# Kernel tuning notes

Hardware: AMD Instinct MI355X
Metric: run time of the kernel (lower is better)

## Reference

```python
import jax, jax.numpy as jnp
import numpy as np

LN_EPS = 1e-5
FACTOR = 4

def layer_norm(x, w, b):
    mu = jnp.mean(x, axis=-1, keepdims=True)
    var = jnp.mean((x - mu) ** 2, axis=-1, keepdims=True)
    return (x - mu) * jax.lax.rsqrt(var + LN_EPS) * w + b

def setup_inputs() -> dict:
    key = jax.random.key(0)
    k1, k2, k3 = jax.random.split(key, 3)
    B, Sq, Skv, D = 4, 2048, 8192, 1024
    return {
        "query": jax.random.normal(k1, (B, Sq, D), dtype=jnp.float32),
        "key": jax.random.normal(k2, (B, Skv, D), dtype=jnp.float32),
        "value": jax.random.normal(k3, (B, Skv, D), dtype=jnp.float32),
        "ln_weight": jnp.ones((D,), dtype=jnp.float32),
        "ln_bias": jnp.zeros((D,), dtype=jnp.float32),
    }

def attention_downsampling(q, k, v, factor):
    # q: [B, S//f, D], k/v: [B, S, D]
    B, S, D = k.shape
    k_win = k.reshape(B, S // factor, factor, D)
    weights = jnp.einsum('bsd,bsfd->bsf', q, k_win).reshape(B, S)  # no softmax
    attn = weights[:, :, None] * v                                  # [B, S, D]
    attn = attn.reshape(B, S // factor, factor, D).sum(axis=2)      # [B, S//f, D]
    return attn

def reference(query, key, value, ln_weight, ln_bias):
    # pre-norm (post_norm=False): residual + attention over normed q/k/v
    qn = layer_norm(query, ln_weight, ln_bias)
    kn = layer_norm(key, ln_weight, ln_bias)
    vn = layer_norm(value, ln_weight, ln_bias)
    return query + attention_downsampling(qn, kn, vn, FACTOR)
```

## Files before the change

kernel.cpp:

```cpp
#include <hip/hip_runtime.h>


constexpr int D      = 1024;
constexpr int FACTOR = 4;
constexpr int BLOCK  = 256;
constexpr int NW     = BLOCK / 64;
constexpr float EPS  = 1e-5f;

__device__ __forceinline__ float wave_reduce_sum(float x) {
#pragma unroll
    for (int off = 32; off > 0; off >>= 1)
        x += __shfl_down(x, off, 64);
    return x;
}

template <int N>
__device__ __forceinline__ void block_reduce(float* vals, float* s_buf) {
    const int lane = threadIdx.x & 63;
    const int wave = threadIdx.x >> 6;
#pragma unroll
    for (int i = 0; i < N; i++) {
        float x = wave_reduce_sum(vals[i]);
        if (lane == 0) s_buf[wave * N + i] = x;
    }
    __syncthreads();
#pragma unroll
    for (int i = 0; i < N; i++) {
        float t = 0.f;
#pragma unroll
        for (int w = 0; w < NW; w++) t += s_buf[w * N + i];
        vals[i] = t;
    }
    __syncthreads();
}

__device__ __forceinline__ float4 ln4(float4 x, float mu, float rs, float4 w, float4 b) {
    float4 r;
    r.x = (x.x - mu) * rs * w.x + b.x;
    r.y = (x.y - mu) * rs * w.y + b.y;
    r.z = (x.z - mu) * rs * w.z + b.z;
    r.w = (x.w - mu) * rs * w.w + b.w;
    return r;
}

__device__ __forceinline__ float dot4(float4 a, float4 b) {
    return a.x * b.x + a.y * b.y + a.z * b.z + a.w * b.w;
}

__global__ __launch_bounds__(BLOCK) void attn_ds_kernel(
    const float* __restrict__ q,
    const float* __restrict__ k,
    const float* __restrict__ v,
    const float* __restrict__ lw,
    const float* __restrict__ lb,
    float* __restrict__ out)
{
    __shared__ float s_buf[NW * 18];

    const size_t row = blockIdx.x;
    const int tid = threadIdx.x;
    const int d0  = tid * 4;

    const float4 qv = *(const float4*)(q + row * D + d0);
    float4 kv[FACTOR], vv[FACTOR];
#pragma unroll
    for (int f = 0; f < FACTOR; f++) {
        kv[f] = *(const float4*)(k + (row * FACTOR + f) * (size_t)D + d0);
        vv[f] = *(const float4*)(v + (row * FACTOR + f) * (size_t)D + d0);
    }
    const float4 wv = *(const float4*)(lw + d0);
    const float4 bv = *(const float4*)(lb + d0);

    float red[18];
    red[0] = qv.x + qv.y + qv.z + qv.w;
    red[1] = qv.x * qv.x + qv.y * qv.y + qv.z * qv.z + qv.w * qv.w;
#pragma unroll
    for (int f = 0; f < FACTOR; f++) {
        red[2 + 2 * f]  = kv[f].x + kv[f].y + kv[f].z + kv[f].w;
        red[3 + 2 * f]  = kv[f].x * kv[f].x + kv[f].y * kv[f].y + kv[f].z * kv[f].z + kv[f].w * kv[f].w;
        red[10 + 2 * f] = vv[f].x + vv[f].y + vv[f].z + vv[f].w;
        red[11 + 2 * f] = vv[f].x * vv[f].x + vv[f].y * vv[f].y + vv[f].z * vv[f].z + vv[f].w * vv[f].w;
    }
    block_reduce<18>(red, s_buf);

    const float invD = 1.0f / (float)D;
    const float mu_q = red[0] * invD;
    const float rs_q = rsqrtf(red[1] * invD - mu_q * mu_q + EPS);
    float mu_k[FACTOR], rs_k[FACTOR], mu_v[FACTOR], rs_v[FACTOR];
#pragma unroll
    for (int f = 0; f < FACTOR; f++) {
        mu_k[f] = red[2 + 2 * f] * invD;
        rs_k[f] = rsqrtf(red[3 + 2 * f] * invD - mu_k[f] * mu_k[f] + EPS);
        mu_v[f] = red[10 + 2 * f] * invD;
        rs_v[f] = rsqrtf(red[11 + 2 * f] * invD - mu_v[f] * mu_v[f] + EPS);
    }

    const float4 qn = ln4(qv, mu_q, rs_q, wv, bv);
    float dp[FACTOR];
#pragma unroll
    for (int f = 0; f < FACTOR; f++) {
        const float4 kn = ln4(kv[f], mu_k[f], rs_k[f], wv, bv);
        dp[f] = dot4(qn, kn);
    }
    block_reduce<FACTOR>(dp, s_buf);

    float4 acc = qv;
#pragma unroll
    for (int f = 0; f < FACTOR; f++) {
        const float4 vn = ln4(vv[f], mu_v[f], rs_v[f], wv, bv);
        acc.x += dp[f] * vn.x;
        acc.y += dp[f] * vn.y;
        acc.z += dp[f] * vn.z;
        acc.w += dp[f] * vn.w;
    }
    *(float4*)(out + row * D + d0) = acc;
}

extern "C" void kernel_launch(void* const* d_in, const int* in_sizes, int n_in,
                              void* d_out, int out_size, void* d_ws, size_t ws_size,
                              hipStream_t stream) {
    const float* q  = (const float*)d_in[0];
    const float* k  = (const float*)d_in[1];
    const float* v  = (const float*)d_in[2];
    const float* lw = (const float*)d_in[3];
    const float* lb = (const float*)d_in[4];
    float* out = (float*)d_out;

    const int rows = in_sizes[0] / D;
    attn_ds_kernel<<<dim3(rows), dim3(BLOCK), 0, stream>>>(q, k, v, lw, lb, out);
}
```

Before: 310.4 us.

## Process one row per wave with DPP reductions and algebraic LN-dot expansion

Each wave now handles a full output row, so block-level shared-memory reductions and barriers are replaced with DPP-based wave reductions. The normalized q·k dot product is computed from raw moment sums (sum, sum of squares, weighted cross terms) instead of materializing normalized vectors. V loads are deferred until after the K statistics are reduced to limit register pressure. The trade-off is much higher per-thread register use, the occupancy hint may cause spills, and the expanded variance formula carries some cancellation risk.

```diff
diff --git a/kernel.cpp b/kernel.cpp
--- a/kernel.cpp
+++ b/kernel.cpp
@@ -1,53 +1,28 @@
 #include <hip/hip_runtime.h>
 
 
-constexpr int D      = 1024;
-constexpr int FACTOR = 4;
-constexpr int BLOCK  = 256;
-constexpr int NW     = BLOCK / 64;
-constexpr float EPS  = 1e-5f;
+constexpr int D     = 1024;
+constexpr int BLOCK = 256;
+constexpr float EPS = 1e-5f;
 
-__device__ __forceinline__ float wave_reduce_sum(float x) {
-#pragma unroll
-    for (int off = 32; off > 0; off >>= 1)
-        x += __shfl_down(x, off, 64);
-    return x;
+template<int CTRL>
+__device__ __forceinline__ float dpp_add(float x) {
+    int xi = __builtin_bit_cast(int, x);
+    int yi = __builtin_amdgcn_update_dpp(0, xi, CTRL, 0xF, 0xF, true);
+    return x + __builtin_bit_cast(float, yi);
 }
 
-template <int N>
-__device__ __forceinline__ void block_reduce(float* vals, float* s_buf) {
-    const int lane = threadIdx.x & 63;
-    const int wave = threadIdx.x >> 6;
-#pragma unroll
-    for (int i = 0; i < N; i++) {
-        float x = wave_reduce_sum(vals[i]);
-        if (lane == 0) s_buf[wave * N + i] = x;
-    }
-    __syncthreads();
-#pragma unroll
-    for (int i = 0; i < N; i++) {
-        float t = 0.f;
-#pragma unroll
-        for (int w = 0; w < NW; w++) t += s_buf[w * N + i];
-        vals[i] = t;
-    }
-    __syncthreads();
+__device__ __forceinline__ float wave_sum(float x) {
+    x = dpp_add<0x111>(x);
+    x = dpp_add<0x112>(x);
+    x = dpp_add<0x114>(x);
+    x = dpp_add<0x118>(x);
+    x = dpp_add<0x142>(x);
+    x = dpp_add<0x143>(x);
+    return __builtin_bit_cast(float, __builtin_amdgcn_readlane(__builtin_bit_cast(int, x), 63));
 }
 
-__device__ __forceinline__ float4 ln4(float4 x, float mu, float rs, float4 w, float4 b) {
-    float4 r;
-    r.x = (x.x - mu) * rs * w.x + b.x;
-    r.y = (x.y - mu) * rs * w.y + b.y;
-    r.z = (x.z - mu) * rs * w.z + b.z;
-    r.w = (x.w - mu) * rs * w.w + b.w;
-    return r;
-}
-
-__device__ __forceinline__ float dot4(float4 a, float4 b) {
-    return a.x * b.x + a.y * b.y + a.z * b.z + a.w * b.w;
-}
-
-__global__ __launch_bounds__(BLOCK) void attn_ds_kernel(
+__global__ __launch_bounds__(BLOCK, 3) void attn_ds_kernel(
     const float* __restrict__ q,
     const float* __restrict__ k,
     const float* __restrict__ v,
@@ -55,65 +30,127 @@
     const float* __restrict__ lb,
     float* __restrict__ out)
 {
-    __shared__ float s_buf[NW * 18];
+    const int lane = threadIdx.x & 63;
+    const int wid  = threadIdx.x >> 6;
+    const long row = (long)blockIdx.x * 4 + wid;
+    const int off0 = lane * 4;
 
-    const size_t row = blockIdx.x;
-    const int tid = threadIdx.x;
-    const int d0  = tid * 4;
+    const float* qp = q + row * D;
+    const float* kp = k + row * (4L * D);
+    const float* vp = v + row * (4L * D);
 
-    const float4 qv = *(const float4*)(q + row * D + d0);
-    float4 kv[FACTOR], vv[FACTOR];
+    float4 qv[4], wv[4], bv[4], kv[4][4];
 #pragma unroll
-    for (int f = 0; f < FACTOR; f++) {
-        kv[f] = *(const float4*)(k + (row * FACTOR + f) * (size_t)D + d0);
-        vv[f] = *(const float4*)(v + (row * FACTOR + f) * (size_t)D + d0);
+    for (int c = 0; c < 4; c++) {
+        const int e = c * 256 + off0;
+        qv[c] = *(const float4*)(qp + e);
+        wv[c] = *(const float4*)(lw + e);
+        bv[c] = *(const float4*)(lb + e);
     }
-    const float4 wv = *(const float4*)(lw + d0);
-    const float4 bv = *(const float4*)(lb + d0);
+#pragma unroll
+    for (int f = 0; f < 4; f++)
+#pragma unroll
+        for (int c = 0; c < 4; c++)
+            kv[f][c] = *(const float4*)(kp + f * D + c * 256 + off0);
 
-    float red[18];
-    red[0] = qv.x + qv.y + qv.z + qv.w;
-    red[1] = qv.x * qv.x + qv.y * qv.y + qv.z * qv.z + qv.w * qv.w;
+    float4 qw[4];
+    float Sq = 0, Sqq = 0, Sq_w2 = 0, Sq_wb = 0, Sw2 = 0, Swb = 0, Sbb = 0;
 #pragma unroll
-    for (int f = 0; f < FACTOR; f++) {
-        red[2 + 2 * f]  = kv[f].x + kv[f].y + kv[f].z + kv[f].w;
-        red[3 + 2 * f]  = kv[f].x * kv[f].x + kv[f].y * kv[f].y + kv[f].z * kv[f].z + kv[f].w * kv[f].w;
-        red[10 + 2 * f] = vv[f].x + vv[f].y + vv[f].z + vv[f].w;
-        red[11 + 2 * f] = vv[f].x * vv[f].x + vv[f].y * vv[f].y + vv[f].z * vv[f].z + vv[f].w * vv[f].w;
+    for (int c = 0; c < 4; c++) {
+#define ACCQ(m) { \
+        float qe = qv[c].m, we = wv[c].m, be = bv[c].m; \
+        float qwe = qe * we; qw[c].m = qwe; \
+        Sq += qe; Sqq = fmaf(qe, qe, Sqq); \
+        Sq_w2 = fmaf(qwe, we, Sq_w2); Sq_wb = fmaf(qwe, be, Sq_wb); \
+        Sw2 = fmaf(we, we, Sw2); Swb = fmaf(we, be, Swb); Sbb = fmaf(be, be, Sbb); }
+        ACCQ(x) ACCQ(y) ACCQ(z) ACCQ(w)
+#undef ACCQ
     }
-    block_reduce<18>(red, s_buf);
+
+    float Sk[4], Skk[4], Sk_w2[4], Sk_wb[4], Sqk[4];
+#pragma unroll
+    for (int f = 0; f < 4; f++) {
+        float s0 = 0, s1 = 0, s2 = 0, s3 = 0, s4 = 0;
+#pragma unroll
+        for (int c = 0; c < 4; c++) {
+#define ACCK(m) { \
+            float ke = kv[f][c].m, we = wv[c].m, be = bv[c].m; \
+            float kwe = ke * we; \
+            s0 += ke; s1 = fmaf(ke, ke, s1); \
+            s2 = fmaf(kwe, we, s2); s3 = fmaf(kwe, be, s3); \
+            s4 = fmaf(qw[c].m, kwe, s4); }
+            ACCK(x) ACCK(y) ACCK(z) ACCK(w)
+#undef ACCK
+        }
+        Sk[f] = s0; Skk[f] = s1; Sk_w2[f] = s2; Sk_wb[f] = s3; Sqk[f] = s4;
+    }
+
+    Sq = wave_sum(Sq);   Sqq = wave_sum(Sqq);
+    Sq_w2 = wave_sum(Sq_w2); Sq_wb = wave_sum(Sq_wb);
+    Sw2 = wave_sum(Sw2); Swb = wave_sum(Swb); Sbb = wave_sum(Sbb);
+#pragma unroll
+    for (int f = 0; f < 4; f++) {
+        Sk[f] = wave_sum(Sk[f]);       Skk[f] = wave_sum(Skk[f]);
+        Sk_w2[f] = wave_sum(Sk_w2[f]); Sk_wb[f] = wave_sum(Sk_wb[f]);
+        Sqk[f] = wave_sum(Sqk[f]);
+    }
+
+    asm volatile("" ::: "memory");
+    float4 vv[4][4];
+#pragma unroll
+    for (int f = 0; f < 4; f++)
+#pragma unroll
+        for (int c = 0; c < 4; c++)
+            vv[f][c] = *(const float4*)(vp + f * D + c * 256 + off0);
 
     const float invD = 1.0f / (float)D;
-    const float mu_q = red[0] * invD;
-    const float rs_q = rsqrtf(red[1] * invD - mu_q * mu_q + EPS);
-    float mu_k[FACTOR], rs_k[FACTOR], mu_v[FACTOR], rs_v[FACTOR];
+    const float mu_q = Sq * invD;
+    const float rs_q = rsqrtf(fmaf(-mu_q, mu_q, Sqq * invD) + EPS);
+    const float qwb_c = Sq_wb - mu_q * Swb;
+    float dp[4];
 #pragma unroll
-    for (int f = 0; f < FACTOR; f++) {
-        mu_k[f] = red[2 + 2 * f] * invD;
-        rs_k[f] = rsqrtf(red[3 + 2 * f] * invD - mu_k[f] * mu_k[f] + EPS);
-        mu_v[f] = red[10 + 2 * f] * invD;
-        rs_v[f] = rsqrtf(red[11 + 2 * f] * invD - mu_v[f] * mu_v[f] + EPS);
+    for (int f = 0; f < 4; f++) {
+        float mu_k = Sk[f] * invD;
+        float rs_k = rsqrtf(fmaf(-mu_k, mu_k, Skk[f] * invD) + EPS);
+        float cross = Sqk[f] - mu_q * Sk_w2[f] - mu_k * Sq_w2 + mu_q * mu_k * Sw2;
+        dp[f] = rs_q * rs_k * cross + rs_q * qwb_c + rs_k * (Sk_wb[f] - mu_k * Swb) + Sbb;
     }
 
-    const float4 qn = ln4(qv, mu_q, rs_q, wv, bv);
-    float dp[FACTOR];
+    float Sv[4], Svv[4];
 #pragma unroll
-    for (int f = 0; f < FACTOR; f++) {
-        const float4 kn = ln4(kv[f], mu_k[f], rs_k[f], wv, bv);
-        dp[f] = dot4(qn, kn);
+    for (int f = 0; f < 4; f++) {
+        float s0 = 0, s1 = 0;
+#pragma unroll
+        for (int c = 0; c < 4; c++) {
+#define ACCV(m) { float ve = vv[f][c].m; s0 += ve; s1 = fmaf(ve, ve, s1); }
+            ACCV(x) ACCV(y) ACCV(z) ACCV(w)
+#undef ACCV
+        }
+        Sv[f] = wave_sum(s0); Svv[f] = wave_sum(s1);
     }
-    block_reduce<FACTOR>(dp, s_buf);
 
-    float4 acc = qv;
+    float4 acc[4];
 #pragma unroll
-    for (int f = 0; f < FACTOR; f++) {
-        const float4 vn = ln4(vv[f], mu_v[f], rs_v[f], wv, bv);
-        acc.x += dp[f] * vn.x;
-        acc.y += dp[f] * vn.y;
-        acc.z += dp[f] * vn.z;
-        acc.w += dp[f] * vn.w;
+    for (int c = 0; c < 4; c++) acc[c] = qv[c];
+#pragma unroll
+    for (int f = 0; f < 4; f++) {
+        float mu_v = Sv[f] * invD;
+        float rs_v = rsqrtf(fmaf(-mu_v, mu_v, Svv[f] * invD) + EPS);
+        float av = rs_v, cv = -mu_v * rs_v;
+        float dpf = dp[f];
+#pragma unroll
+        for (int c = 0; c < 4; c++) {
+#define ACCO(m) { \
+            float t = fmaf(av, vv[f][c].m, cv); \
+            float vn = fmaf(t, wv[c].m, bv[c].m); \
+            acc[c].m = fmaf(dpf, vn, acc[c].m); }
+            ACCO(x) ACCO(y) ACCO(z) ACCO(w)
+#undef ACCO
+        }
     }
-    *(float4*)(out + row * D + d0) = acc;
+#pragma unroll
+    for (int c = 0; c < 4; c++)
+        *(float4*)(out + row * D + c * 256 + off0) = acc[c];
 }
 
 extern "C" void kernel_launch(void* const* d_in, const int* in_sizes, int n_in,
@@ -127,5 +164,5 @@
     float* out = (float*)d_out;
 
     const int rows = in_sizes[0] / D;
-    attn_ds_kernel<<<dim3(rows), dim3(BLOCK), 0, stream>>>(q, k, v, lw, lb, out);
+    attn_ds_kernel<<<dim3(rows / 4), dim3(BLOCK), 0, stream>>>(q, k, v, lw, lb, out);
 }
```

Result: no change. 310.2 us (-0.1%).

## Stage K/V rows into LDS via direct global-to-LDS loads, use DPP reductions

Applied to the files above, without the earlier changes.

K and V rows for each output row are no longer loaded into registers with per-thread float4 loads. They are copied straight into a 32 KB LDS buffer with global_load_lds, then read back from LDS after a barrier. The aim is to issue the large K/V reads as wide DMA-style transfers with fewer VGPRs and better coalescing. Wave reductions now use DPP row and broadcast adds plus a readlane instead of shuffle-down chains, and the layer-norm arithmetic is recast as fmaf. The LDS allocation may limit blocks per CU, and correctness relies on the barrier waiting for the LDS-bound loads to complete.

```diff
diff --git a/kernel.cpp b/kernel.cpp
--- a/kernel.cpp
+++ b/kernel.cpp
@@ -1,27 +1,38 @@
 #include <hip/hip_runtime.h>
 
 
-constexpr int D      = 1024;
-constexpr int FACTOR = 4;
-constexpr int BLOCK  = 256;
-constexpr int NW     = BLOCK / 64;
-constexpr float EPS  = 1e-5f;
+constexpr int D     = 1024;
+constexpr int BLOCK = 256;
+constexpr int NW    = BLOCK / 64;
+constexpr float EPS = 1e-5f;
 
-__device__ __forceinline__ float wave_reduce_sum(float x) {
-#pragma unroll
-    for (int off = 32; off > 0; off >>= 1)
-        x += __shfl_down(x, off, 64);
-    return x;
+#define GLOBAL_AS const __attribute__((address_space(1))) void*
+#define LDS_AS __attribute__((address_space(3))) void*
+
+template<int CTRL>
+__device__ __forceinline__ float dpp_add(float x) {
+    int xi = __builtin_bit_cast(int, x);
+    int yi = __builtin_amdgcn_update_dpp(0, xi, CTRL, 0xF, 0xF, true);
+    return x + __builtin_bit_cast(float, yi);
+}
+
+__device__ __forceinline__ float wave_sum(float x) {
+    x = dpp_add<0x111>(x);
+    x = dpp_add<0x112>(x);
+    x = dpp_add<0x114>(x);
+    x = dpp_add<0x118>(x);
+    x = dpp_add<0x142>(x);
+    x = dpp_add<0x143>(x);
+    return __builtin_bit_cast(float, __builtin_amdgcn_readlane(__builtin_bit_cast(int, x), 63));
 }
 
 template <int N>
-__device__ __forceinline__ void block_reduce(float* vals, float* s_buf) {
-    const int lane = threadIdx.x & 63;
-    const int wave = threadIdx.x >> 6;
+__device__ __forceinline__ void block_reduce(float* vals, float* s_buf,
+                                             int lane, int wid) {
 #pragma unroll
     for (int i = 0; i < N; i++) {
-        float x = wave_reduce_sum(vals[i]);
-        if (lane == 0) s_buf[wave * N + i] = x;
+        float x = wave_sum(vals[i]);
+        if (lane == 0) s_buf[wid * N + i] = x;
     }
     __syncthreads();
 #pragma unroll
@@ -34,19 +45,6 @@
     __syncthreads();
 }
 
-__device__ __forceinline__ float4 ln4(float4 x, float mu, float rs, float4 w, float4 b) {
-    float4 r;
-    r.x = (x.x - mu) * rs * w.x + b.x;
-    r.y = (x.y - mu) * rs * w.y + b.y;
-    r.z = (x.z - mu) * rs * w.z + b.z;
-    r.w = (x.w - mu) * rs * w.w + b.w;
-    return r;
-}
-
-__device__ __forceinline__ float dot4(float4 a, float4 b) {
-    return a.x * b.x + a.y * b.y + a.z * b.z + a.w * b.w;
-}
-
 __global__ __launch_bounds__(BLOCK) void attn_ds_kernel(
     const float* __restrict__ q,
     const float* __restrict__ k,
@@ -55,63 +53,87 @@
     const float* __restrict__ lb,
     float* __restrict__ out)
 {
+    __shared__ float kv_lds[8 * D];
     __shared__ float s_buf[NW * 18];
 
-    const size_t row = blockIdx.x;
-    const int tid = threadIdx.x;
-    const int d0  = tid * 4;
+    const long row  = blockIdx.x;
+    const int  tid  = threadIdx.x;
+    const int  lane = tid & 63;
+    const int  wid  = tid >> 6;
+    const int  d0   = tid * 4;
 
     const float4 qv = *(const float4*)(q + row * D + d0);
-    float4 kv[FACTOR], vv[FACTOR];
-#pragma unroll
-    for (int f = 0; f < FACTOR; f++) {
-        kv[f] = *(const float4*)(k + (row * FACTOR + f) * (size_t)D + d0);
-        vv[f] = *(const float4*)(v + (row * FACTOR + f) * (size_t)D + d0);
-    }
     const float4 wv = *(const float4*)(lw + d0);
     const float4 bv = *(const float4*)(lb + d0);
+
+    const float* kbase = k + row * (4L * D);
+    const float* vbase = v + row * (4L * D);
+#pragma unroll
+    for (int i = 0; i < 8; i++) {
+        const int c = wid + i * NW;
+        const float* src = (c < 16 ? kbase : vbase) + (long)(c & 15) * 256 + lane * 4;
+        float* dst = kv_lds + c * 256;
+        __builtin_amdgcn_global_load_lds((GLOBAL_AS)src, (LDS_AS)dst, 16, 0, 0);
+    }
+
+    __syncthreads();
 
     float red[18];
     red[0] = qv.x + qv.y + qv.z + qv.w;
     red[1] = qv.x * qv.x + qv.y * qv.y + qv.z * qv.z + qv.w * qv.w;
+    float4 kv4[4], vv4[4];
 #pragma unroll
-    for (int f = 0; f < FACTOR; f++) {
-        red[2 + 2 * f]  = kv[f].x + kv[f].y + kv[f].z + kv[f].w;
-        red[3 + 2 * f]  = kv[f].x * kv[f].x + kv[f].y * kv[f].y + kv[f].z * kv[f].z + kv[f].w * kv[f].w;
-        red[10 + 2 * f] = vv[f].x + vv[f].y + vv[f].z + vv[f].w;
-        red[11 + 2 * f] = vv[f].x * vv[f].x + vv[f].y * vv[f].y + vv[f].z * vv[f].z + vv[f].w * vv[f].w;
+    for (int f = 0; f < 4; f++) {
+        kv4[f] = *(const float4*)(kv_lds + f * D + d0);
+        vv4[f] = *(const float4*)(kv_lds + (4 + f) * D + d0);
+        red[2 + 2 * f]  = kv4[f].x + kv4[f].y + kv4[f].z + kv4[f].w;
+        red[3 + 2 * f]  = kv4[f].x * kv4[f].x + kv4[f].y * kv4[f].y
+                        + kv4[f].z * kv4[f].z + kv4[f].w * kv4[f].w;
+        red[10 + 2 * f] = vv4[f].x + vv4[f].y + vv4[f].z + vv4[f].w;
+        red[11 + 2 * f] = vv4[f].x * vv4[f].x + vv4[f].y * vv4[f].y
+                        + vv4[f].z * vv4[f].z + vv4[f].w * vv4[f].w;
     }
-    block_reduce<18>(red, s_buf);
+    block_reduce<18>(red, s_buf, lane, wid);
 
     const float invD = 1.0f / (float)D;
     const float mu_q = red[0] * invD;
-    const float rs_q = rsqrtf(red[1] * invD - mu_q * mu_q + EPS);
-    float mu_k[FACTOR], rs_k[FACTOR], mu_v[FACTOR], rs_v[FACTOR];
+    const float rs_q = rsqrtf(fmaf(-mu_q, mu_q, red[1] * invD) + EPS);
+    float mu_k[4], rs_k[4], mu_v[4], rs_v[4];
 #pragma unroll
-    for (int f = 0; f < FACTOR; f++) {
+    for (int f = 0; f < 4; f++) {
         mu_k[f] = red[2 + 2 * f] * invD;
-        rs_k[f] = rsqrtf(red[3 + 2 * f] * invD - mu_k[f] * mu_k[f] + EPS);
+        rs_k[f] = rsqrtf(fmaf(-mu_k[f], mu_k[f], red[3 + 2 * f] * invD) + EPS);
         mu_v[f] = red[10 + 2 * f] * invD;
-        rs_v[f] = rsqrtf(red[11 + 2 * f] * invD - mu_v[f] * mu_v[f] + EPS);
+        rs_v[f] = rsqrtf(fmaf(-mu_v[f], mu_v[f], red[11 + 2 * f] * invD) + EPS);
     }
 
-    const float4 qn = ln4(qv, mu_q, rs_q, wv, bv);
-    float dp[FACTOR];
+    float4 qn;
+    qn.x = fmaf((qv.x - mu_q) * rs_q, wv.x, bv.x);
+    qn.y = fmaf((qv.y - mu_q) * rs_q, wv.y, bv.y);
+    qn.z = fmaf((qv.z - mu_q) * rs_q, wv.z, bv.z);
+    qn.w = fmaf((qv.w - mu_q) * rs_q, wv.w, bv.w);
+    float dp[4];
 #pragma unroll
-    for (int f = 0; f < FACTOR; f++) {
-        const float4 kn = ln4(kv[f], mu_k[f], rs_k[f], wv, bv);
-        dp[f] = dot4(qn, kn);
+    for (int f = 0; f < 4; f++) {
+        float4 kn;
+        kn.x = fmaf((kv4[f].x - mu_k[f]) * rs_k[f], wv.x, bv.x);
+        kn.y = fmaf((kv4[f].y - mu_k[f]) * rs_k[f], wv.y, bv.y);
+        kn.z = fmaf((kv4[f].z - mu_k[f]) * rs_k[f], wv.z, bv.z);
+        kn.w = fmaf((kv4[f].w - mu_k[f]) * rs_k[f], wv.w, bv.w);
+        dp[f] = qn.x * kn.x + qn.y * kn.y + qn.z * kn.z + qn.w * kn.w;
     }
-    block_reduce<FACTOR>(dp, s_buf);
+    block_reduce<4>(dp, s_buf, lane, wid);
 
     float4 acc = qv;
 #pragma unroll
-    for (int f = 0; f < FACTOR; f++) {
-        const float4 vn = ln4(vv[f], mu_v[f], rs_v[f], wv, bv);
-        acc.x += dp[f] * vn.x;
-        acc.y += dp[f] * vn.y;
-        acc.z += dp[f] * vn.z;
-        acc.w += dp[f] * vn.w;
+    for (int f = 0; f < 4; f++) {
+        const float av = rs_v[f], cv = -mu_v[f] * rs_v[f], dpf = dp[f];
+#define ACCO(m) { \
+        float t  = fmaf(av, vv4[f].m, cv); \
+        float vn = fmaf(t, wv.m, bv.m); \
+        acc.m = fmaf(dpf, vn, acc.m); }
+        ACCO(x) ACCO(y) ACCO(z) ACCO(w)
+#undef ACCO
     }
     *(float4*)(out + row * D + d0) = acc;
 }
```

New measurement: 306.5 us. No clear change (-1.3%).
